# Performance work log

Hardware: AMD Instinct MI355X
Metric: run time of the kernel (lower is better)

The kernel has to match this reference:

```python
import jax, jax.numpy as jnp
import numpy as np

NUM_SPEAKERS = 8192  # static stand-in for labels.max()+1
MARGIN = 0.2
EPS = 1e-12  # torch F.normalize default eps


def _l2_normalize(x, axis=1):
    norm = jnp.linalg.norm(x, axis=axis, keepdims=True)
    return x / jnp.maximum(norm, EPS)


def setup_inputs() -> dict:
    key = jax.random.key(0)
    k1, k2 = jax.random.split(key)
    embeddings = jax.random.normal(k1, (8192, 256), dtype=jnp.float32)
    labels = jax.random.randint(k2, (8192,), 0, NUM_SPEAKERS, dtype=jnp.int32)
    return {"embeddings": embeddings, "labels": labels}


def reference(embeddings, labels):
    # Normalize embeddings: [B, D]
    e = _l2_normalize(embeddings, axis=1)
    B = e.shape[0]

    # Scatter-mean prototypes per speaker (replaces the python for-loop):
    sums = jax.ops.segment_sum(e, labels, num_segments=NUM_SPEAKERS)          # [S, D]
    counts = jax.ops.segment_sum(jnp.ones((B,), e.dtype), labels,
                                 num_segments=NUM_SPEAKERS)                    # [S]
    protos = sums / jnp.maximum(counts, 1.0)[:, None]  # zero rows stay zero like torch skip
    protos = _l2_normalize(protos, axis=1)

    # Cosine similarity: [B, S]
    cos_sim = jnp.matmul(e, protos.T)

    # Positive similarity at target column: [B]
    positive_sim = jnp.take_along_axis(cos_sim, labels[:, None].astype(jnp.int32), axis=1)[:, 0]

    # Faithful to original: subtract margin on the diagonal (requires B == S)
    cos_sim_m = cos_sim - MARGIN * jnp.eye(NUM_SPEAKERS, dtype=cos_sim.dtype)
    negative_sim = jnp.max(cos_sim_m, axis=1)

    loss = jnp.mean(jax.nn.relu(negative_sim - positive_sim + MARGIN))
    return loss
```

## Files before the change

kernel.cpp:

```cpp
#include <hip/hip_runtime.h>
#include <hip/hip_bf16.h>

typedef __attribute__((ext_vector_type(8))) short short8;
typedef __attribute__((ext_vector_type(4))) float f32x4;

#define B_ROWS 8192
#define DIM 256
#define CS 8
#define NT 16
#define NSLICE (CS * 2)
#define MARGIN_F 0.2f
#define BUCKET_CAP 32

__device__ __forceinline__ unsigned short f2bf(float x) {
  unsigned int u = __float_as_uint(x);
  unsigned int r = (u + 0x7fffu + ((u >> 16) & 1u)) >> 16;
  return (unsigned short)r;
}
__device__ __forceinline__ float bf2f(unsigned short h) {
  return __uint_as_float(((unsigned int)h) << 16);
}

__device__ __forceinline__ void gload_lds16(const void* g, void* l) {
  __builtin_amdgcn_global_load_lds(
      (const __attribute__((address_space(1))) unsigned int*)g,
      (__attribute__((address_space(3))) unsigned int*)l, 16, 0, 0);
}

__global__ __launch_bounds__(256) void k_norm_index(
    const float* __restrict__ emb, const int* __restrict__ labels,
    unsigned short* __restrict__ ebf, int* __restrict__ cursor,
    int* __restrict__ bucket) {
  int wid = threadIdx.x >> 6, lane = threadIdx.x & 63;
  int row = blockIdx.x * 4 + wid;
  const float4 v = *reinterpret_cast<const float4*>(emb + row * DIM + lane * 4);
  float ss = v.x * v.x + v.y * v.y + v.z * v.z + v.w * v.w;
#pragma unroll
  for (int off = 32; off > 0; off >>= 1) ss += __shfl_xor(ss, off);
  float scale = 1.0f / fmaxf(sqrtf(ss), 1e-12f);
  ushort4 ob;
  ob.x = f2bf(v.x * scale); ob.y = f2bf(v.y * scale);
  ob.z = f2bf(v.z * scale); ob.w = f2bf(v.w * scale);
  *reinterpret_cast<ushort4*>(ebf + row * DIM + lane * 4) = ob;
  if (lane == 0) {
    int lab = labels[row];
    int slot = atomicAdd(cursor + lab, 1);
    if (slot < BUCKET_CAP) bucket[lab * BUCKET_CAP + slot] = row;
  }
}

__global__ __launch_bounds__(256) void k_protos_gather(
    const unsigned short* __restrict__ ebf, const int* __restrict__ cursor,
    const int* __restrict__ bucket, unsigned short* __restrict__ pbf) {
  int wid = threadIdx.x >> 6, lane = threadIdx.x & 63;
  int s = blockIdx.x * 4 + wid;
  int c = cursor[s];
  if (c > BUCKET_CAP) c = BUCKET_CAP;
  float a0 = 0.f, a1 = 0.f, a2 = 0.f, a3 = 0.f;
  for (int k = 0; k < c; ++k) {
    int row = bucket[s * BUCKET_CAP + k];
    ushort4 ev = *reinterpret_cast<const ushort4*>(ebf + row * DIM + lane * 4);
    a0 += bf2f(ev.x); a1 += bf2f(ev.y); a2 += bf2f(ev.z); a3 += bf2f(ev.w);
  }
  float ss = a0 * a0 + a1 * a1 + a2 * a2 + a3 * a3;
#pragma unroll
  for (int off = 32; off > 0; off >>= 1) ss += __shfl_xor(ss, off);
  float scale = 1.0f / fmaxf(sqrtf(ss), 1e-12f);
  ushort4 ob;
  ob.x = f2bf(a0 * scale); ob.y = f2bf(a1 * scale);
  ob.z = f2bf(a2 * scale); ob.w = f2bf(a3 * scale);
  *reinterpret_cast<ushort4*>(pbf + s * DIM + lane * 4) = ob;
}

__global__ __launch_bounds__(256) void k_pos(
    const unsigned short* __restrict__ ebf, const unsigned short* __restrict__ pbf,
    const int* __restrict__ labels, float* __restrict__ pos) {
  int wid = threadIdx.x >> 6, lane = threadIdx.x & 63;
  int row = blockIdx.x * 4 + wid;
  int lab = labels[row];
  ushort4 ev = *reinterpret_cast<const ushort4*>(ebf + row * DIM + lane * 4);
  ushort4 pv = *reinterpret_cast<const ushort4*>(pbf + lab * DIM + lane * 4);
  float d = bf2f(ev.x) * bf2f(pv.x) + bf2f(ev.y) * bf2f(pv.y) +
            bf2f(ev.z) * bf2f(pv.z) + bf2f(ev.w) * bf2f(pv.w);
#pragma unroll
  for (int off = 32; off > 0; off >>= 1) d += __shfl_xor(d, off);
  if (lane == 0) pos[row] = d;
}

__global__ __attribute__((amdgpu_flat_work_group_size(256, 256)))
__attribute__((amdgpu_waves_per_eu(2, 2))) void k_gemm_negmax(
    const unsigned short* __restrict__ E, const unsigned short* __restrict__ P,
    float* __restrict__ negp) {
  __shared__ unsigned short smbuf[2][32 * 512];
  const int tid = threadIdx.x;
  const int lane = tid & 63, wid = tid >> 6;
  const int l16 = lane & 15, lk = lane >> 4;
  const int wr = (wid >> 1) * 64;
  const int wch = wid & 1;
  const int rowBase = blockIdx.x * 128;
  const int colBase0 = blockIdx.y * 1024;

  auto stageB = [&](int buf, int colTile) {
#pragma unroll
    for (int it = 0; it < 8; ++it) {
      int c = it * 4 + wid;
      int prow = colTile + ((c >> 4) << 5) + (((c >> 3) & 1) << 4) + l16;
      int pel = ((c & 7) << 5) + (lk << 3);
      gload_lds16(P + prow * DIM + pel, &smbuf[buf][c * 512 + lane * 8]);
    }
  };

  stageB(0, colBase0);

  short8 areg[4][8];
#pragma unroll
  for (int m = 0; m < 4; ++m)
#pragma unroll
    for (int ks = 0; ks < 8; ++ks)
      areg[m][ks] = *reinterpret_cast<const short8*>(
          E + (rowBase + wr + m * 16 + l16) * DIM + ks * 32 + lk * 8);

  float rmax[4][4];
#pragma unroll
  for (int m = 0; m < 4; ++m)
#pragma unroll
    for (int r = 0; r < 4; ++r) rmax[m][r] = -3.0e38f;

  __syncthreads();

  for (int ct = 0; ct < NT; ++ct) {
    if (ct + 1 < NT) stageB((ct + 1) & 1, colBase0 + (ct + 1) * 64);

    const unsigned short* bs = smbuf[ct & 1];
    f32x4 acc[4][2] = {};
#pragma unroll
    for (int ks = 0; ks < 8; ++ks) {
      short8 b[2];
#pragma unroll
      for (int n = 0; n < 2; ++n)
        b[n] = *reinterpret_cast<const short8*>(
            bs + ((wch * 2 + n) * 8 + ks) * 512 + lane * 8);
#pragma unroll
      for (int m = 0; m < 4; ++m)
#pragma unroll
        for (int n = 0; n < 2; ++n)
          acc[m][n] = __builtin_amdgcn_mfma_f32_16x16x32_bf16(
              areg[m][ks], b[n], acc[m][n], 0, 0, 0);
    }

    const int colT = colBase0 + ct * 64 + wch * 32;
#pragma unroll
    for (int m = 0; m < 4; ++m) {
      int growb = rowBase + wr + m * 16 + lk * 4;
#pragma unroll
      for (int n = 0; n < 2; ++n) {
        int gcol = colT + n * 16 + l16;
#pragma unroll
        for (int r = 0; r < 4; ++r) {
          float v = acc[m][n][r];
          if (growb + r == gcol) v -= MARGIN_F;
          rmax[m][r] = fmaxf(rmax[m][r], v);
        }
      }
    }

    __syncthreads();
  }

  const int slice = blockIdx.y * 2 + wch;
#pragma unroll
  for (int m = 0; m < 4; ++m) {
#pragma unroll
    for (int r = 0; r < 4; ++r) {
      float v = rmax[m][r];
      v = fmaxf(v, __shfl_xor(v, 1));
      v = fmaxf(v, __shfl_xor(v, 2));
      v = fmaxf(v, __shfl_xor(v, 4));
      v = fmaxf(v, __shfl_xor(v, 8));
      if (l16 == 0) {
        int grow = rowBase + wr + m * 16 + lk * 4 + r;
        negp[slice * B_ROWS + grow] = v;
      }
    }
  }
}

__global__ __launch_bounds__(256) void k_loss_part(
    const float* __restrict__ negp, const float* __restrict__ pos,
    float* __restrict__ out) {
  int i = blockIdx.x * 256 + threadIdx.x;
  float n = negp[i];
#pragma unroll
  for (int s = 1; s < NSLICE; ++s) n = fmaxf(n, negp[s * B_ROWS + i]);
  float t = fmaxf(n - pos[i] + MARGIN_F, 0.f);
#pragma unroll
  for (int off = 32; off > 0; off >>= 1) t += __shfl_xor(t, off);
  __shared__ float red[4];
  if ((threadIdx.x & 63) == 0) red[threadIdx.x >> 6] = t;
  __syncthreads();
  if (threadIdx.x == 0)
    atomicAdd(out, (red[0] + red[1] + red[2] + red[3]) * (1.0f / B_ROWS));
}

extern "C" void kernel_launch(void* const* d_in, const int* in_sizes, int n_in,
                              void* d_out, int out_size, void* d_ws, size_t ws_size,
                              hipStream_t stream) {
  const float* emb = (const float*)d_in[0];
  const int* labels = (const int*)d_in[1];

  char* ws = (char*)d_ws;
  int* cursor = (int*)ws;
  int* bucket = (int*)(ws + 32 * 1024);
  unsigned short* ebf =
      (unsigned short*)(ws + 32 * 1024 + 1024 * 1024);
  unsigned short* pbf =
      (unsigned short*)(ws + 32 * 1024 + 5 * 1024 * 1024);
  float* pos = (float*)(ws + 32 * 1024 + 9 * 1024 * 1024);
  float* negp = (float*)(ws + 64 * 1024 + 9 * 1024 * 1024);

  hipMemsetAsync(cursor, 0, 32 * 1024, stream);
  hipMemsetAsync(d_out, 0, sizeof(float), stream);
  k_norm_index<<<B_ROWS / 4, 256, 0, stream>>>(emb, labels, ebf, cursor, bucket);
  k_protos_gather<<<B_ROWS / 4, 256, 0, stream>>>(ebf, cursor, bucket, pbf);
  k_pos<<<B_ROWS / 4, 256, 0, stream>>>(ebf, pbf, labels, pos);
  k_gemm_negmax<<<dim3(64, CS), 256, 0, stream>>>(ebf, pbf, negp);
  k_loss_part<<<32, 256, 0, stream>>>(negp, pos, (float*)d_out);
}
```

Measured before the change: 116.8 us.

## Fuse positive-sim into prototype kernel, pre-swizzle prototypes, single-block loss reduction

The prototype kernel now computes positive similarities for each bucket member directly, which removes the separate k_pos launch. It also writes prototypes in a fragment-ordered layout, so the GEMM can stage B tiles with contiguous 16-byte loads. The loss reduction moves to a single block that writes the result directly, dropping one memset and the atomic. The trade-offs are a second pass over the bucket rows in the gather kernel and a serial single-block final reduction.

Measured after the change: 121.2 us. +3.8%, slower.

```diff
diff --git a/kernel.cpp b/kernel.cpp
--- a/kernel.cpp
+++ b/kernel.cpp
@@ -51,14 +51,15 @@
 
 __global__ __launch_bounds__(256) void k_protos_gather(
     const unsigned short* __restrict__ ebf, const int* __restrict__ cursor,
-    const int* __restrict__ bucket, unsigned short* __restrict__ pbf) {
+    const int* __restrict__ bucket, unsigned short* __restrict__ pfrag,
+    float* __restrict__ pos) {
   int wid = threadIdx.x >> 6, lane = threadIdx.x & 63;
-  int s = blockIdx.x * 4 + wid;
-  int c = cursor[s];
+  int p = blockIdx.x * 4 + wid;
+  int c = cursor[p];
   if (c > BUCKET_CAP) c = BUCKET_CAP;
   float a0 = 0.f, a1 = 0.f, a2 = 0.f, a3 = 0.f;
   for (int k = 0; k < c; ++k) {
-    int row = bucket[s * BUCKET_CAP + k];
+    int row = bucket[p * BUCKET_CAP + k];
     ushort4 ev = *reinterpret_cast<const ushort4*>(ebf + row * DIM + lane * 4);
     a0 += bf2f(ev.x); a1 += bf2f(ev.y); a2 += bf2f(ev.z); a3 += bf2f(ev.w);
   }
@@ -69,27 +70,24 @@
   ushort4 ob;
   ob.x = f2bf(a0 * scale); ob.y = f2bf(a1 * scale);
   ob.z = f2bf(a2 * scale); ob.w = f2bf(a3 * scale);
-  *reinterpret_cast<ushort4*>(pbf + s * DIM + lane * 4) = ob;
-}
-
-__global__ __launch_bounds__(256) void k_pos(
-    const unsigned short* __restrict__ ebf, const unsigned short* __restrict__ pbf,
-    const int* __restrict__ labels, float* __restrict__ pos) {
-  int wid = threadIdx.x >> 6, lane = threadIdx.x & 63;
-  int row = blockIdx.x * 4 + wid;
-  int lab = labels[row];
-  ushort4 ev = *reinterpret_cast<const ushort4*>(ebf + row * DIM + lane * 4);
-  ushort4 pv = *reinterpret_cast<const ushort4*>(pbf + lab * DIM + lane * 4);
-  float d = bf2f(ev.x) * bf2f(pv.x) + bf2f(ev.y) * bf2f(pv.y) +
-            bf2f(ev.z) * bf2f(pv.z) + bf2f(ev.w) * bf2f(pv.w);
-#pragma unroll
-  for (int off = 32; off > 0; off >>= 1) d += __shfl_xor(d, off);
-  if (lane == 0) pos[row] = d;
+  int addr = (p >> 6) * 16384 + ((((p >> 4) & 3) * 8 + (lane >> 3)) * 512) +
+             ((((lane >> 1) & 3) * 16 + (p & 15)) * 8) + ((lane & 1) * 4);
+  *reinterpret_cast<ushort4*>(pfrag + addr) = ob;
+  float p0 = bf2f(ob.x), p1 = bf2f(ob.y), p2 = bf2f(ob.z), p3 = bf2f(ob.w);
+  for (int k = 0; k < c; ++k) {
+    int row = bucket[p * BUCKET_CAP + k];
+    ushort4 ev = *reinterpret_cast<const ushort4*>(ebf + row * DIM + lane * 4);
+    float d = bf2f(ev.x) * p0 + bf2f(ev.y) * p1 + bf2f(ev.z) * p2 +
+              bf2f(ev.w) * p3;
+#pragma unroll
+    for (int off = 32; off > 0; off >>= 1) d += __shfl_xor(d, off);
+    if (lane == 0) pos[row] = d;
+  }
 }
 
 __global__ __attribute__((amdgpu_flat_work_group_size(256, 256)))
 __attribute__((amdgpu_waves_per_eu(2, 2))) void k_gemm_negmax(
-    const unsigned short* __restrict__ E, const unsigned short* __restrict__ P,
+    const unsigned short* __restrict__ E, const unsigned short* __restrict__ PF,
     float* __restrict__ negp) {
   __shared__ unsigned short smbuf[2][32 * 512];
   const int tid = threadIdx.x;
@@ -99,18 +97,18 @@
   const int wch = wid & 1;
   const int rowBase = blockIdx.x * 128;
   const int colBase0 = blockIdx.y * 1024;
-
-  auto stageB = [&](int buf, int colTile) {
+  const int tile0 = blockIdx.y * NT;
+
+  auto stageB = [&](int buf, int tile) {
 #pragma unroll
     for (int it = 0; it < 8; ++it) {
       int c = it * 4 + wid;
-      int prow = colTile + ((c >> 4) << 5) + (((c >> 3) & 1) << 4) + l16;
-      int pel = ((c & 7) << 5) + (lk << 3);
-      gload_lds16(P + prow * DIM + pel, &smbuf[buf][c * 512 + lane * 8]);
+      gload_lds16(PF + tile * 16384 + c * 512 + lane * 8,
+                  &smbuf[buf][c * 512 + lane * 8]);
     }
   };
 
-  stageB(0, colBase0);
+  stageB(0, tile0);
 
   short8 areg[4][8];
 #pragma unroll
@@ -129,7 +127,7 @@
   __syncthreads();
 
   for (int ct = 0; ct < NT; ++ct) {
-    if (ct + 1 < NT) stageB((ct + 1) & 1, colBase0 + (ct + 1) * 64);
+    if (ct + 1 < NT) stageB((ct + 1) & 1, tile0 + ct + 1);
 
     const unsigned short* bs = smbuf[ct & 1];
     f32x4 acc[4][2] = {};
@@ -185,21 +183,23 @@
   }
 }
 
-__global__ __launch_bounds__(256) void k_loss_part(
+__global__ __launch_bounds__(256) void k_loss(
     const float* __restrict__ negp, const float* __restrict__ pos,
     float* __restrict__ out) {
-  int i = blockIdx.x * 256 + threadIdx.x;
-  float n = negp[i];
-#pragma unroll
-  for (int s = 1; s < NSLICE; ++s) n = fmaxf(n, negp[s * B_ROWS + i]);
-  float t = fmaxf(n - pos[i] + MARGIN_F, 0.f);
-#pragma unroll
-  for (int off = 32; off > 0; off >>= 1) t += __shfl_xor(t, off);
+  int tid = threadIdx.x;
+  float s = 0.f;
+  for (int i = tid; i < B_ROWS; i += 256) {
+    float n = negp[i];
+#pragma unroll
+    for (int sl = 1; sl < NSLICE; ++sl) n = fmaxf(n, negp[sl * B_ROWS + i]);
+    s += fmaxf(n - pos[i] + MARGIN_F, 0.f);
+  }
+#pragma unroll
+  for (int off = 32; off > 0; off >>= 1) s += __shfl_xor(s, off);
   __shared__ float red[4];
-  if ((threadIdx.x & 63) == 0) red[threadIdx.x >> 6] = t;
+  if ((tid & 63) == 0) red[tid >> 6] = s;
   __syncthreads();
-  if (threadIdx.x == 0)
-    atomicAdd(out, (red[0] + red[1] + red[2] + red[3]) * (1.0f / B_ROWS));
+  if (tid == 0) out[0] = (red[0] + red[1] + red[2] + red[3]) * (1.0f / B_ROWS);
 }
 
 extern "C" void kernel_launch(void* const* d_in, const int* in_sizes, int n_in,
@@ -213,16 +213,14 @@
   int* bucket = (int*)(ws + 32 * 1024);
   unsigned short* ebf =
       (unsigned short*)(ws + 32 * 1024 + 1024 * 1024);
-  unsigned short* pbf =
+  unsigned short* pfrag =
       (unsigned short*)(ws + 32 * 1024 + 5 * 1024 * 1024);
   float* pos = (float*)(ws + 32 * 1024 + 9 * 1024 * 1024);
   float* negp = (float*)(ws + 64 * 1024 + 9 * 1024 * 1024);
 
   hipMemsetAsync(cursor, 0, 32 * 1024, stream);
-  hipMemsetAsync(d_out, 0, sizeof(float), stream);
   k_norm_index<<<B_ROWS / 4, 256, 0, stream>>>(emb, labels, ebf, cursor, bucket);
-  k_protos_gather<<<B_ROWS / 4, 256, 0, stream>>>(ebf, cursor, bucket, pbf);
-  k_pos<<<B_ROWS / 4, 256, 0, stream>>>(ebf, pbf, labels, pos);
-  k_gemm_negmax<<<dim3(64, CS), 256, 0, stream>>>(ebf, pbf, negp);
-  k_loss_part<<<32, 256, 0, stream>>>(negp, pos, (float*)d_out);
-}
+  k_protos_gather<<<B_ROWS / 4, 256, 0, stream>>>(ebf, cursor, bucket, pfrag, pos);
+  k_gemm_negmax<<<dim3(64, CS), 256, 0, stream>>>(ebf, pfrag, negp);
+  k_loss<<<1, 256, 0, stream>>>(negp, pos, (float*)d_out);
+}
```
